# Optimization experiments

Hardware: AMD Instinct MI355X
Metric: run time of the kernel (lower is better)

## Reference

```python
import jax, jax.numpy as jnp
import numpy as np
import math

D_MODEL = 768
N_HEAD = 12
HEAD_DIM = D_MODEL // N_HEAD
B = 4
W = 32
HW = W * W


def setup_inputs() -> dict:
    key = jax.random.key(0)
    k1, k2, k3 = jax.random.split(key, 3)
    x = jax.random.normal(k1, (B, HW, D_MODEL), dtype=jnp.float32)
    w_qkv = jax.random.normal(k2, (3 * D_MODEL, D_MODEL), dtype=jnp.float32) * (D_MODEL ** -0.5)
    w_out = jax.random.normal(k3, (D_MODEL, D_MODEL), dtype=jnp.float32) * (D_MODEL ** -0.5)
    gamma = jnp.ones((D_MODEL,), dtype=jnp.float32)
    return {"x": x, "w_qkv": w_qkv, "w_out": w_out, "gamma": gamma}


def _axial_sincos(w, head_dim, dtype):
    # Axial RoPE: first half of head_dim encodes row position, second half column.
    dim_half = head_dim // 2
    inv_freq = 1.0 / (10000.0 ** (jnp.arange(0, dim_half, 2, dtype=dtype) / dim_half))  # (dim_half//2,)
    pos = jnp.arange(w, dtype=dtype)
    ang = pos[:, None] * inv_freq[None, :]                 # (w, f)
    row = jnp.repeat(ang[:, None, :], w, axis=1)           # (w, w, f)
    col = jnp.repeat(ang[None, :, :], w, axis=0)           # (w, w, f)
    theta = jnp.concatenate([row, col], axis=-1).reshape(w * w, dim_half)  # (hw, head_dim//2)
    theta = jnp.concatenate([theta, theta], axis=-1)       # rotate-half layout -> (hw, head_dim)
    return jnp.sin(theta), jnp.cos(theta)


def _rotate_half(t):
    t1, t2 = jnp.split(t, 2, axis=-1)
    return jnp.concatenate([-t2, t1], axis=-1)


def _apply_rotary(t, sin, cos):
    return t * cos + _rotate_half(t) * sin


def _rms_norm(x, gamma, eps=1e-6):
    return x * jax.lax.rsqrt(jnp.mean(x * x, axis=-1, keepdims=True) + eps) * gamma


def _attn_mask(w):
    # Faithful to the torch source: mask[center, neighbor] = False, else True.
    # torch SDPA bool semantics: True = attend. So 3x3 neighbors are EXCLUDED.
    idx = jnp.arange(w * w)
    r, c = idx // w, idx % w
    neighbor = (jnp.abs(r[:, None] - r[None, :]) <= 1) & (jnp.abs(c[:, None] - c[None, :]) <= 1)
    return ~neighbor  # (hw, hw) bool, True = allowed


def reference(x, w_qkv, w_out, gamma):
    Bx, hw, d = x.shape
    w = int(math.isqrt(hw))
    h, hd = N_HEAD, HEAD_DIM
    sin, cos = _axial_sincos(w, hd, x.dtype)               # (hw, hd) each
    xn = _rms_norm(x, gamma)
    qkv = xn @ w_qkv.T                                     # (B, hw, 3d)
    qkv = qkv.reshape(Bx, hw, 3, h, hd)
    q = jnp.transpose(qkv[:, :, 0], (0, 2, 1, 3))          # (B, h, hw, hd)
    k = jnp.transpose(qkv[:, :, 1], (0, 2, 1, 3))
    v = jnp.transpose(qkv[:, :, 2], (0, 2, 1, 3))
    q = _apply_rotary(q, sin, cos)
    k = _apply_rotary(k, sin, cos)
    allow = _attn_mask(w)
    scale = 1.0 / jnp.sqrt(jnp.asarray(hd, x.dtype))
    scores = jnp.einsum('bhid,bhjd->bhij', q, k) * scale   # (B, h, hw, hw)
    scores = jnp.where(allow[None, None], scores, jnp.asarray(-jnp.inf, x.dtype))
    probs = jax.nn.softmax(scores, axis=-1)
    out = jnp.einsum('bhij,bhjd->bhid', probs, v)          # (B, h, hw, hd)
    out = jnp.transpose(out, (0, 2, 1, 3)).reshape(Bx, hw, d)
    return out @ w_out.T
```

## Files before the change

kernel.cpp:

```cpp
#include <hip/hip_runtime.h>

typedef __attribute__((ext_vector_type(8))) short short8;
typedef __attribute__((ext_vector_type(4))) float f32x4;
typedef __attribute__((ext_vector_type(4))) unsigned short ushort4_t;
typedef unsigned short ushort_t;
typedef unsigned long long u64;

#define D_MODEL 768
#define NHEAD 12
#define HD 64
#define BATCH 4
#define HWIDTH 32
#define HW 1024
#define TOK (BATCH*HW)
#define QKV_N (3*D_MODEL)
#define BH (BATCH*NHEAD)
#define QSCALE 0.18033688f

__device__ __forceinline__ ushort_t f2bf(float f) {
    union { float f; unsigned u; } v; v.f = f;
    unsigned u = v.u;
    unsigned r = u + 0x7FFFu + ((u >> 16) & 1u);
    return (ushort_t)(r >> 16);
}
__device__ __forceinline__ float bf2f(ushort_t h) {
    union { unsigned u; float f; } v; v.u = ((unsigned)h) << 16;
    return v.f;
}
__device__ __forceinline__ float ex2(float x) {
    float r; asm("v_exp_f32 %0, %1" : "=v"(r) : "v"(x)); return r;
}
__device__ __forceinline__ unsigned cvtpk(float lo, float hi) {
    unsigned r; asm("v_cvt_pk_bf16_f32 %0, %1, %2" : "=v"(r) : "v"(lo), "v"(hi)); return r;
}

__global__ void rmsnorm_kernel(const float* __restrict__ x, const float* __restrict__ gamma,
                               ushort_t* __restrict__ xn) {
    int wave = threadIdx.x >> 6, lane = threadIdx.x & 63;
    int t = blockIdx.x * 4 + wave;
    const float* xr = x + (size_t)t * D_MODEL;
    float v[12]; float ss = 0.f;
    #pragma unroll
    for (int j = 0; j < 12; ++j) { v[j] = xr[lane + j*64]; ss += v[j]*v[j]; }
    #pragma unroll
    for (int m = 1; m < 64; m <<= 1) ss += __shfl_xor(ss, m, 64);
    float r = rsqrtf(ss * (1.f/768.f) + 1e-6f);
    ushort_t* o = xn + (size_t)t * D_MODEL;
    #pragma unroll
    for (int j = 0; j < 12; ++j) o[lane + j*64] = f2bf(v[j] * r * gamma[lane + j*64]);
}

__global__ void cvt_kernel(const float* __restrict__ in, ushort_t* __restrict__ out, int n) {
    int i = blockIdx.x * blockDim.x + threadIdx.x;
    if (i < n) out[i] = f2bf(in[i]);
}

__global__ void sincos_kernel(float* __restrict__ sint, float* __restrict__ cost) {
    int i = blockIdx.x * blockDim.x + threadIdx.x;
    int p = i >> 5, j = i & 31;
    int r = p >> 5, c = p & 31;
    int jj = j & 15;
    float freq = powf(10000.f, -(float)(2*jj) / 32.f);
    float pos = (j < 16) ? (float)r : (float)c;
    float th = pos * freq;
    sint[i] = sinf(th);
    cost[i] = cosf(th);
}

template<int NTILES, int EPI>
__global__ __launch_bounds__(256, 2) void gemm128(const ushort_t* __restrict__ A,
                                                  const ushort_t* __restrict__ B,
                                                  const float* __restrict__ sint,
                                                  const float* __restrict__ cost,
                                                  ushort_t* __restrict__ Qr,
                                                  ushort_t* __restrict__ Kr,
                                                  ushort_t* __restrict__ VTt,
                                                  float* __restrict__ C) {
    __shared__ ushort_t As[2][128*64];
    __shared__ ushort_t Bs[2][128*64];
    const int K = 768;
    constexpr int NR = NTILES / 2;
    int c = blockIdx.x & 7;
    int l = blockIdx.x >> 3;
    int mtile = (c >> 1)*8 + l / NR;
    int ntile = (c & 1)*NR + l % NR;
    int tm = mtile * 128, tn = ntile * 128;
    int w = threadIdx.x >> 6, lane = threadIdx.x & 63;
    int wr = w >> 1, wc = w & 1;
    int l15 = lane & 15, l4 = lane >> 4;

    const ushort_t* mat = (w < 2) ? A : B;
    int mbase = (w < 2) ? tm : tn;
    ushort_t* lds_half = (w < 2) ? &As[0][0] : &Bs[0][0];
    int r0w = (w & 1) * 64;
    int srow = r0w + (lane >> 3);
    int sslot = (lane & 7) ^ (srow & 7);
    const ushort_t* gsrc0 = mat + (size_t)(mbase + srow)*K + sslot*8;

    auto stage = [&](int buf, int kstep) {
        int k0 = kstep * 64;
        #pragma unroll
        for (int j = 0; j < 8; ++j) {
            const ushort_t* g = gsrc0 + (size_t)(j*8)*K + k0;
            __builtin_amdgcn_global_load_lds((const __attribute__((address_space(1))) void*)g,
                (__attribute__((address_space(3))) void*)(lds_half + (size_t)buf*8192 + (r0w + j*8)*64),
                16, 0, 0);
        }
    };

    f32x4 acc[4][4] = {};
    auto compute = [&](int bi) {
        short8 af[4][2], bfx[4][2];
        #pragma unroll
        for (int mi = 0; mi < 4; ++mi) {
            int row = wr*64 + mi*16 + l15;
            #pragma unroll
            for (int kk = 0; kk < 2; ++kk)
                af[mi][kk] = *(const short8*)&As[bi][row*64 + ((kk*4 + l4) ^ (row & 7))*8];
        }
        #pragma unroll
        for (int ni = 0; ni < 4; ++ni) {
            int row = wc*64 + ni*16 + l15;
            #pragma unroll
            for (int kk = 0; kk < 2; ++kk)
                bfx[ni][kk] = *(const short8*)&Bs[bi][row*64 + ((kk*4 + l4) ^ (row & 7))*8];
        }
        #pragma unroll
        for (int kk = 0; kk < 2; ++kk)
            #pragma unroll
            for (int mi = 0; mi < 4; ++mi)
                #pragma unroll
                for (int ni = 0; ni < 4; ++ni)
                    acc[mi][ni] = __builtin_amdgcn_mfma_f32_16x16x32_bf16(af[mi][kk], bfx[ni][kk], acc[mi][ni], 0, 0, 0);
    };

    stage(0, 0); stage(1, 1);
    for (int t = 0; t < 12; ++t) {
        if (t < 11) { asm volatile("s_waitcnt vmcnt(8)" ::: "memory"); }
        else        { asm volatile("s_waitcnt vmcnt(0)" ::: "memory"); }
        __builtin_amdgcn_s_barrier();
        compute(t & 1);
        __builtin_amdgcn_s_barrier();
        if (t < 10) stage(t & 1, t + 2);
    }

    if constexpr (EPI == 0) {
        int col_base = tn + wc*64;
        int region = col_base / 768;
        int h = (col_base % 768) >> 6;
        if (region < 2) {
            ushort_t* dst = (region == 0) ? Qr : Kr;
            float scale = (region == 0) ? QSCALE : 1.f;
            #pragma unroll
            for (int mi = 0; mi < 4; ++mi) {
                #pragma unroll
                for (int ni = 0; ni < 2; ++ni) {
                    int d = ni*16 + l15;
                    #pragma unroll
                    for (int r = 0; r < 4; ++r) {
                        int pt = tm + wr*64 + mi*16 + l4*4 + r;
                        int b = pt >> 10, p = pt & 1023;
                        float s = sint[p*32 + d], cc = cost[p*32 + d];
                        float t0 = acc[mi][ni][r], t1 = acc[mi][ni+2][r];
                        size_t o = (size_t)(b*NHEAD + h)*HW*HD + (size_t)p*HD + d;
                        dst[o]      = f2bf((t0*cc - t1*s) * scale);
                        dst[o + 32] = f2bf((t1*cc + t0*s) * scale);
                    }
                }
            }
        } else {
            #pragma unroll
            for (int mi = 0; mi < 4; ++mi) {
                int pt = tm + wr*64 + mi*16 + l4*4;
                int b = pt >> 10, p = pt & 1023;
                size_t hb = (size_t)(b*NHEAD + h)*HD*HW;
                #pragma unroll
                for (int ni = 0; ni < 4; ++ni) {
                    int d = ni*16 + l15;
                    ushort4_t pk;
                    pk.x = f2bf(acc[mi][ni][0]);
                    pk.y = f2bf(acc[mi][ni][1]);
                    pk.z = f2bf(acc[mi][ni][2]);
                    pk.w = f2bf(acc[mi][ni][3]);
                    *(ushort4_t*)&VTt[hb + (size_t)d*HW + p] = pk;
                }
            }
        }
    } else {
        #pragma unroll
        for (int mi = 0; mi < 4; ++mi)
            #pragma unroll
            for (int ni = 0; ni < 4; ++ni)
                #pragma unroll
                for (int r = 0; r < 4; ++r) {
                    int row = tm + wr*64 + mi*16 + l4*4 + r;
                    int col = tn + wc*64 + ni*16 + l15;
                    C[(size_t)row*(128*NTILES) + col] = acc[mi][ni][r];
                }
    }
}

__global__ __launch_bounds__(256) void attn_kernel(const ushort_t* __restrict__ Q,
                                                   const ushort_t* __restrict__ Kt,
                                                   const ushort_t* __restrict__ VT,
                                                   ushort_t* __restrict__ Ao) {
    __shared__ ushort_t Kb[2][64*64];
    __shared__ ushort_t Vb[2][64*64];
    __shared__ ushort_t P[4][16][72];
    int flat = blockIdx.x;
    int swz = (flat & 7) * 96 + (flat >> 3);
    int bh = swz >> 4;
    int qtile = swz & 15;
    int w = threadIdx.x >> 6, lane = threadIdx.x & 63;
    int l15 = lane & 15, l4 = lane >> 4;
    int qbase = qtile * 64 + w * 16;
    int q = qbase + l15;
    int qr = q >> 5, qc = q & 31;
    const ushort_t* Qh = Q + (size_t)bh * HW * HD;
    const ushort_t* Kh = Kt + (size_t)bh * HW * HD;
    const ushort_t* Vh = VT + (size_t)bh * HD * HW;
    short8 aq0 = *(const short8*)&Qh[(size_t)q*64 + l4*8];
    short8 aq1 = *(const short8*)&Qh[(size_t)q*64 + 32 + l4*8];
    unsigned pat = (qc == 0) ? 3u : (7u << (qc - 1));
    float m = -1e30f, lsum = 0.f;
    f32x4 oacc[4] = {};

    auto stage = [&](int bufi, int kv) {
        #pragma unroll
        for (int is = 0; is < 2; ++is) {
            int c = is*256 + w*64 + lane;
            int row = c >> 3;
            int col16 = (c & 7) ^ (row & 7);
            const ushort_t* ga = Kh + (size_t)(kv + row)*64 + col16*8;
            __builtin_amdgcn_global_load_lds((const __attribute__((address_space(1))) void*)ga,
                (__attribute__((address_space(3))) void*)(&Kb[bufi][(size_t)(is*256 + w*64)*8]), 16, 0, 0);
            const ushort_t* gv = Vh + (size_t)row*HW + kv + col16*8;
            __builtin_amdgcn_global_load_lds((const __attribute__((address_space(1))) void*)gv,
                (__attribute__((address_space(3))) void*)(&Vb[bufi][(size_t)(is*256 + w*64)*8]), 16, 0, 0);
        }
    };

    stage(0, 0); stage(1, 64);

    for (int t = 0; t < 16; ++t) {
        if (t < 15) { asm volatile("s_waitcnt vmcnt(4)" ::: "memory"); }
        else        { asm volatile("s_waitcnt vmcnt(0)" ::: "memory"); }
        __builtin_amdgcn_s_barrier();
        int cur = t & 1;
        int kv = t * 64;
        int sw = l15 & 7;
        f32x4 s[4];
        #pragma unroll
        for (int st = 0; st < 4; ++st) {
            int krow = st*16 + l15;
            short8 bk0 = *(const short8*)&Kb[cur][(size_t)krow*64 + (size_t)((l4 ^ sw))*8];
            short8 bk1 = *(const short8*)&Kb[cur][(size_t)krow*64 + (size_t)(((4+l4) ^ sw))*8];
            f32x4 z = {};
            z = __builtin_amdgcn_mfma_f32_16x16x32_bf16(bk0, aq0, z, 0, 0, 0);
            z = __builtin_amdgcn_mfma_f32_16x16x32_bf16(bk1, aq1, z, 0, 0, 0);
            s[st] = z;
        }
        short8 va0[4], va1[4];
        #pragma unroll
        for (int dt = 0; dt < 4; ++dt) {
            int vrow = dt*16 + l15;
            va0[dt] = *(const short8*)&Vb[cur][(size_t)vrow*64 + (size_t)((l4 ^ sw))*8];
            va1[dt] = *(const short8*)&Vb[cur][(size_t)vrow*64 + (size_t)(((4+l4) ^ sw))*8];
        }
        int dr = qr - (kv >> 5);
        if (dr >= -1 && dr <= 2) {
            u64 tm = 0;
            if (dr <= 1) tm |= (u64)pat;
            if (dr >= 0) tm |= ((u64)pat) << 32;
            u64 sub = tm >> (l4*4);
            #pragma unroll
            for (int st = 0; st < 4; ++st)
                #pragma unroll
                for (int i = 0; i < 4; ++i)
                    if ((sub >> (st*16 + i)) & 1) s[st][i] = -1e30f;
        }
        float vmax = fmaxf(
            fmaxf(fmaxf(fmaxf(s[0][0], s[0][1]), fmaxf(s[0][2], s[0][3])),
                  fmaxf(fmaxf(s[1][0], s[1][1]), fmaxf(s[1][2], s[1][3]))),
            fmaxf(fmaxf(fmaxf(s[2][0], s[2][1]), fmaxf(s[2][2], s[2][3])),
                  fmaxf(fmaxf(s[3][0], s[3][1]), fmaxf(s[3][2], s[3][3]))));
        vmax = fmaxf(vmax, __shfl_xor(vmax, 16, 64));
        vmax = fmaxf(vmax, __shfl_xor(vmax, 32, 64));
        if (__any(vmax - m > 8.f)) {
            float mn = fmaxf(m, vmax);
            float sf = ex2(m - mn);
            lsum *= sf;
            #pragma unroll
            for (int dt = 0; dt < 4; ++dt)
                #pragma unroll
                for (int i = 0; i < 4; ++i) oacc[dt][i] *= sf;
            m = mn;
        }
        float ls = 0.f;
        #pragma unroll
        for (int st = 0; st < 4; ++st) {
            float p0 = ex2(s[st][0] - m), p1 = ex2(s[st][1] - m);
            float p2 = ex2(s[st][2] - m), p3 = ex2(s[st][3] - m);
            ls += (p0 + p1) + (p2 + p3);
            uint2 pk;
            pk.x = cvtpk(p0, p1);
            pk.y = cvtpk(p2, p3);
            *(uint2*)&P[w][l15][st*16 + l4*4] = pk;
        }
        ls += __shfl_xor(ls, 16, 64);
        ls += __shfl_xor(ls, 32, 64);
        lsum += ls;
        short8 pf0 = *(const short8*)&P[w][l15][l4*8];
        short8 pf1 = *(const short8*)&P[w][l15][32 + l4*8];
        #pragma unroll
        for (int dt = 0; dt < 4; ++dt) {
            oacc[dt] = __builtin_amdgcn_mfma_f32_16x16x32_bf16(va0[dt], pf0, oacc[dt], 0, 0, 0);
            oacc[dt] = __builtin_amdgcn_mfma_f32_16x16x32_bf16(va1[dt], pf1, oacc[dt], 0, 0, 0);
        }
        __builtin_amdgcn_s_barrier();
        if (t < 14) stage(cur, (t + 2) * 64);
    }
    int b = bh / NHEAD, h = bh % NHEAD;
    float rl = 1.f / lsum;
    size_t obase = ((size_t)b*HW + q)*D_MODEL + h*64;
    #pragma unroll
    for (int dt = 0; dt < 4; ++dt) {
        uint2 pk;
        pk.x = cvtpk(oacc[dt][0]*rl, oacc[dt][1]*rl);
        pk.y = cvtpk(oacc[dt][2]*rl, oacc[dt][3]*rl);
        *(uint2*)&Ao[obase + dt*16 + l4*4] = pk;
    }
}

extern "C" void kernel_launch(void* const* d_in, const int* in_sizes, int n_in,
                              void* d_out, int out_size, void* d_ws, size_t ws_size,
                              hipStream_t stream) {
    const float* x      = (const float*)d_in[0];
    const float* w_qkv  = (const float*)d_in[1];
    const float* w_out  = (const float*)d_in[2];
    const float* gamma  = (const float*)d_in[3];
    float* out = (float*)d_out;

    char* ws = (char*)d_ws;
    size_t off = 0;
    auto alloc = [&](size_t bytes) { char* p = ws + off; off += (bytes + 255) & ~255ull; return p; };
    ushort_t* xn   = (ushort_t*)alloc((size_t)TOK*D_MODEL*2);
    ushort_t* wq   = (ushort_t*)alloc((size_t)QKV_N*D_MODEL*2);
    ushort_t* wo   = (ushort_t*)alloc((size_t)D_MODEL*D_MODEL*2);
    float* sint    = (float*)alloc((size_t)HW*32*4);
    float* cost    = (float*)alloc((size_t)HW*32*4);
    ushort_t* Qr   = (ushort_t*)alloc((size_t)BH*HW*HD*2);
    ushort_t* Kr   = (ushort_t*)alloc((size_t)BH*HW*HD*2);
    ushort_t* VTt  = (ushort_t*)alloc((size_t)BH*HD*HW*2);
    ushort_t* Ao   = (ushort_t*)alloc((size_t)TOK*D_MODEL*2);

    rmsnorm_kernel<<<TOK/4, 256, 0, stream>>>(x, gamma, xn);
    cvt_kernel<<<(QKV_N*D_MODEL + 255)/256, 256, 0, stream>>>(w_qkv, wq, QKV_N*D_MODEL);
    cvt_kernel<<<(D_MODEL*D_MODEL + 255)/256, 256, 0, stream>>>(w_out, wo, D_MODEL*D_MODEL);
    sincos_kernel<<<HW*32/256, 256, 0, stream>>>(sint, cost);
    gemm128<18,0><<<576, 256, 0, stream>>>(xn, wq, sint, cost, Qr, Kr, VTt, nullptr);
    attn_kernel<<<768, 256, 0, stream>>>(Qr, Kr, VTt, Ao);
    gemm128<6,1><<<192, 256, 0, stream>>>(Ao, wo, nullptr, nullptr, nullptr, nullptr, nullptr, out);
}
```

Measured before the change: 80.10 us.

## Split attention KV into two halves with combine pass, fuse prep kernels, reorder GEMM pipeline

Merges the rmsnorm, weight-conversion and sincos kernels into one prep launch, with float4-vectorised weight conversion. Attention is now split over two halves of the key range, each using 32-key tiles, and a new combine kernel merges the partial outputs and (max, sum) pairs. This doubles the block count and raises occupancy through smaller LDS tiles and launch_bounds(256,6), and adds setprio around the MFMAs. The GEMM and attention loops now read their LDS fragments first, then issue the next prefetch before the MFMAs to overlap loads with compute. The cost is extra fp32 partial traffic and one more kernel launch.

After: 82.22 us. 2.6% more time.

```diff
diff --git a/kernel.cpp b/kernel.cpp
--- a/kernel.cpp
+++ b/kernel.cpp
@@ -4,7 +4,6 @@
 typedef __attribute__((ext_vector_type(4))) float f32x4;
 typedef __attribute__((ext_vector_type(4))) unsigned short ushort4_t;
 typedef unsigned short ushort_t;
-typedef unsigned long long u64;
 
 #define D_MODEL 768
 #define NHEAD 12
@@ -23,10 +22,6 @@
     unsigned r = u + 0x7FFFu + ((u >> 16) & 1u);
     return (ushort_t)(r >> 16);
 }
-__device__ __forceinline__ float bf2f(ushort_t h) {
-    union { unsigned u; float f; } v; v.u = ((unsigned)h) << 16;
-    return v.f;
-}
 __device__ __forceinline__ float ex2(float x) {
     float r; asm("v_exp_f32 %0, %1" : "=v"(r) : "v"(x)); return r;
 }
@@ -34,37 +29,50 @@
     unsigned r; asm("v_cvt_pk_bf16_f32 %0, %1, %2" : "=v"(r) : "v"(lo), "v"(hi)); return r;
 }
 
-__global__ void rmsnorm_kernel(const float* __restrict__ x, const float* __restrict__ gamma,
-                               ushort_t* __restrict__ xn) {
-    int wave = threadIdx.x >> 6, lane = threadIdx.x & 63;
-    int t = blockIdx.x * 4 + wave;
-    const float* xr = x + (size_t)t * D_MODEL;
-    float v[12]; float ss = 0.f;
-    #pragma unroll
-    for (int j = 0; j < 12; ++j) { v[j] = xr[lane + j*64]; ss += v[j]*v[j]; }
-    #pragma unroll
-    for (int m = 1; m < 64; m <<= 1) ss += __shfl_xor(ss, m, 64);
-    float r = rsqrtf(ss * (1.f/768.f) + 1e-6f);
-    ushort_t* o = xn + (size_t)t * D_MODEL;
-    #pragma unroll
-    for (int j = 0; j < 12; ++j) o[lane + j*64] = f2bf(v[j] * r * gamma[lane + j*64]);
-}
-
-__global__ void cvt_kernel(const float* __restrict__ in, ushort_t* __restrict__ out, int n) {
-    int i = blockIdx.x * blockDim.x + threadIdx.x;
-    if (i < n) out[i] = f2bf(in[i]);
-}
-
-__global__ void sincos_kernel(float* __restrict__ sint, float* __restrict__ cost) {
-    int i = blockIdx.x * blockDim.x + threadIdx.x;
-    int p = i >> 5, j = i & 31;
-    int r = p >> 5, c = p & 31;
-    int jj = j & 15;
-    float freq = powf(10000.f, -(float)(2*jj) / 32.f);
-    float pos = (j < 16) ? (float)r : (float)c;
-    float th = pos * freq;
-    sint[i] = sinf(th);
-    cost[i] = cosf(th);
+__global__ __launch_bounds__(256) void prep_kernel(const float* __restrict__ x,
+                                                   const float* __restrict__ gamma,
+                                                   ushort_t* __restrict__ xn,
+                                                   const float* __restrict__ w_qkv,
+                                                   ushort_t* __restrict__ wq,
+                                                   const float* __restrict__ w_out,
+                                                   ushort_t* __restrict__ wo,
+                                                   float* __restrict__ sint,
+                                                   float* __restrict__ cost) {
+    int blk = blockIdx.x;
+    if (blk < 1024) {
+        int wave = threadIdx.x >> 6, lane = threadIdx.x & 63;
+        int t = blk * 4 + wave;
+        const float* xr = x + (size_t)t * D_MODEL;
+        float v[12]; float ss = 0.f;
+        #pragma unroll
+        for (int j = 0; j < 12; ++j) { v[j] = xr[lane + j*64]; ss += v[j]*v[j]; }
+        #pragma unroll
+        for (int m = 1; m < 64; m <<= 1) ss += __shfl_xor(ss, m, 64);
+        float r = rsqrtf(ss * (1.f/768.f) + 1e-6f);
+        ushort_t* o = xn + (size_t)t * D_MODEL;
+        #pragma unroll
+        for (int j = 0; j < 12; ++j) o[lane + j*64] = f2bf(v[j] * r * gamma[lane + j*64]);
+    } else if (blk < 2752) {
+        int i = (blk - 1024) * 1024 + threadIdx.x * 4;
+        float4 v = *(const float4*)&w_qkv[i];
+        uint2 pk; pk.x = cvtpk(v.x, v.y); pk.y = cvtpk(v.z, v.w);
+        *(uint2*)&wq[i] = pk;
+    } else if (blk < 3328) {
+        int i = (blk - 2752) * 1024 + threadIdx.x * 4;
+        float4 v = *(const float4*)&w_out[i];
+        uint2 pk; pk.x = cvtpk(v.x, v.y); pk.y = cvtpk(v.z, v.w);
+        *(uint2*)&wo[i] = pk;
+    } else {
+        int i = (blk - 3328) * 256 + threadIdx.x;
+        int p = i >> 5, j = i & 31;
+        int r = p >> 5, c = p & 31;
+        int jj = j & 15;
+        float freq = powf(10000.f, -(float)(2*jj) / 32.f);
+        float pos = (j < 16) ? (float)r : (float)c;
+        float th = pos * freq;
+        sint[i] = sinf(th);
+        cost[i] = cosf(th);
+    }
 }
 
 template<int NTILES, int EPI>
@@ -109,39 +117,37 @@
     };
 
     f32x4 acc[4][4] = {};
-    auto compute = [&](int bi) {
-        short8 af[4][2], bfx[4][2];
-        #pragma unroll
-        for (int mi = 0; mi < 4; ++mi) {
-            int row = wr*64 + mi*16 + l15;
-            #pragma unroll
-            for (int kk = 0; kk < 2; ++kk)
-                af[mi][kk] = *(const short8*)&As[bi][row*64 + ((kk*4 + l4) ^ (row & 7))*8];
-        }
-        #pragma unroll
-        for (int ni = 0; ni < 4; ++ni) {
-            int row = wc*64 + ni*16 + l15;
-            #pragma unroll
-            for (int kk = 0; kk < 2; ++kk)
-                bfx[ni][kk] = *(const short8*)&Bs[bi][row*64 + ((kk*4 + l4) ^ (row & 7))*8];
-        }
-        #pragma unroll
-        for (int kk = 0; kk < 2; ++kk)
-            #pragma unroll
-            for (int mi = 0; mi < 4; ++mi)
-                #pragma unroll
-                for (int ni = 0; ni < 4; ++ni)
-                    acc[mi][ni] = __builtin_amdgcn_mfma_f32_16x16x32_bf16(af[mi][kk], bfx[ni][kk], acc[mi][ni], 0, 0, 0);
-    };
-
     stage(0, 0); stage(1, 1);
     for (int t = 0; t < 12; ++t) {
         if (t < 11) { asm volatile("s_waitcnt vmcnt(8)" ::: "memory"); }
         else        { asm volatile("s_waitcnt vmcnt(0)" ::: "memory"); }
         __builtin_amdgcn_s_barrier();
-        compute(t & 1);
+        int bi = t & 1;
+        short8 af[4][2], bfx[4][2];
+        #pragma unroll
+        for (int mi = 0; mi < 4; ++mi) {
+            int row = wr*64 + mi*16 + l15;
+            #pragma unroll
+            for (int kk = 0; kk < 2; ++kk)
+                af[mi][kk] = *(const short8*)&As[bi][row*64 + ((kk*4 + l4) ^ (row & 7))*8];
+        }
+        #pragma unroll
+        for (int ni = 0; ni < 4; ++ni) {
+            int row = wc*64 + ni*16 + l15;
+            #pragma unroll
+            for (int kk = 0; kk < 2; ++kk)
+                bfx[ni][kk] = *(const short8*)&Bs[bi][row*64 + ((kk*4 + l4) ^ (row & 7))*8];
+        }
+        asm volatile("s_waitcnt lgkmcnt(0)" ::: "memory");
         __builtin_amdgcn_s_barrier();
-        if (t < 10) stage(t & 1, t + 2);
+        if (t < 10) stage(bi, t + 2);
+        #pragma unroll
+        for (int kk = 0; kk < 2; ++kk)
+            #pragma unroll
+            for (int mi = 0; mi < 4; ++mi)
+                #pragma unroll
+                for (int ni = 0; ni < 4; ++ni)
+                    acc[mi][ni] = __builtin_amdgcn_mfma_f32_16x16x32_bf16(af[mi][kk], bfx[ni][kk], acc[mi][ni], 0, 0, 0);
     }
 
     if constexpr (EPI == 0) {
@@ -200,22 +206,21 @@
     }
 }
 
-__global__ __launch_bounds__(256) void attn_kernel(const ushort_t* __restrict__ Q,
-                                                   const ushort_t* __restrict__ Kt,
-                                                   const ushort_t* __restrict__ VT,
-                                                   ushort_t* __restrict__ Ao) {
-    __shared__ ushort_t Kb[2][64*64];
-    __shared__ ushort_t Vb[2][64*64];
-    __shared__ ushort_t P[4][16][72];
-    int flat = blockIdx.x;
-    int swz = (flat & 7) * 96 + (flat >> 3);
-    int bh = swz >> 4;
-    int qtile = swz & 15;
+__global__ __launch_bounds__(256, 6) void attn_kernel(const ushort_t* __restrict__ Q,
+                                                      const ushort_t* __restrict__ Kt,
+                                                      const ushort_t* __restrict__ VT,
+                                                      float* __restrict__ Opart,
+                                                      float2* __restrict__ Ml) {
+    __shared__ ushort_t Kb[2][32*64];
+    __shared__ ushort_t Vb[2][64*32];
+    __shared__ ushort_t P[4][16][40];
+    int qtile = blockIdx.x, bh = blockIdx.y, split = blockIdx.z;
     int w = threadIdx.x >> 6, lane = threadIdx.x & 63;
     int l15 = lane & 15, l4 = lane >> 4;
     int qbase = qtile * 64 + w * 16;
     int q = qbase + l15;
-    int qr = q >> 5, qc = q & 31;
+    int qr = qbase >> 5;
+    int qc = q & 31;
     const ushort_t* Qh = Q + (size_t)bh * HW * HD;
     const ushort_t* Kh = Kt + (size_t)bh * HW * HD;
     const ushort_t* Vh = VT + (size_t)bh * HD * HW;
@@ -224,66 +229,67 @@
     unsigned pat = (qc == 0) ? 3u : (7u << (qc - 1));
     float m = -1e30f, lsum = 0.f;
     f32x4 oacc[4] = {};
-
+    int kv0 = split * 512;
+
+    int krow_s = w*8 + (lane >> 3);
+    int kslot_s = (lane & 7) ^ (lane >> 3);
+    int vrow_s = w*16 + (lane >> 2);
+    int vslot_s = (lane & 3) ^ (vrow_s & 3) ^ ((vrow_s >> 2) & 3);
     auto stage = [&](int bufi, int kv) {
-        #pragma unroll
-        for (int is = 0; is < 2; ++is) {
-            int c = is*256 + w*64 + lane;
-            int row = c >> 3;
-            int col16 = (c & 7) ^ (row & 7);
-            const ushort_t* ga = Kh + (size_t)(kv + row)*64 + col16*8;
-            __builtin_amdgcn_global_load_lds((const __attribute__((address_space(1))) void*)ga,
-                (__attribute__((address_space(3))) void*)(&Kb[bufi][(size_t)(is*256 + w*64)*8]), 16, 0, 0);
-            const ushort_t* gv = Vh + (size_t)row*HW + kv + col16*8;
-            __builtin_amdgcn_global_load_lds((const __attribute__((address_space(1))) void*)gv,
-                (__attribute__((address_space(3))) void*)(&Vb[bufi][(size_t)(is*256 + w*64)*8]), 16, 0, 0);
-        }
+        const ushort_t* ga = Kh + (size_t)(kv + krow_s)*64 + kslot_s*8;
+        __builtin_amdgcn_global_load_lds((const __attribute__((address_space(1))) void*)ga,
+            (__attribute__((address_space(3))) void*)(&Kb[bufi][w*512]), 16, 0, 0);
+        const ushort_t* gv = Vh + (size_t)vrow_s*HW + kv + vslot_s*8;
+        __builtin_amdgcn_global_load_lds((const __attribute__((address_space(1))) void*)gv,
+            (__attribute__((address_space(3))) void*)(&Vb[bufi][w*512]), 16, 0, 0);
     };
 
-    stage(0, 0); stage(1, 64);
+    stage(0, kv0); stage(1, kv0 + 32);
 
     for (int t = 0; t < 16; ++t) {
-        if (t < 15) { asm volatile("s_waitcnt vmcnt(4)" ::: "memory"); }
+        if (t < 15) { asm volatile("s_waitcnt vmcnt(2)" ::: "memory"); }
         else        { asm volatile("s_waitcnt vmcnt(0)" ::: "memory"); }
         __builtin_amdgcn_s_barrier();
         int cur = t & 1;
-        int kv = t * 64;
-        int sw = l15 & 7;
-        f32x4 s[4];
-        #pragma unroll
-        for (int st = 0; st < 4; ++st) {
+        int kv = kv0 + t * 32;
+        short8 bk[2][2];
+        #pragma unroll
+        for (int st = 0; st < 2; ++st) {
             int krow = st*16 + l15;
-            short8 bk0 = *(const short8*)&Kb[cur][(size_t)krow*64 + (size_t)((l4 ^ sw))*8];
-            short8 bk1 = *(const short8*)&Kb[cur][(size_t)krow*64 + (size_t)(((4+l4) ^ sw))*8];
-            f32x4 z = {};
-            z = __builtin_amdgcn_mfma_f32_16x16x32_bf16(bk0, aq0, z, 0, 0, 0);
-            z = __builtin_amdgcn_mfma_f32_16x16x32_bf16(bk1, aq1, z, 0, 0, 0);
-            s[st] = z;
-        }
-        short8 va0[4], va1[4];
+            bk[st][0] = *(const short8*)&Kb[cur][krow*64 + ((l4 ^ (krow & 7)))*8];
+            bk[st][1] = *(const short8*)&Kb[cur][krow*64 + (((4 + l4) ^ (krow & 7)))*8];
+        }
+        short8 va[4];
         #pragma unroll
         for (int dt = 0; dt < 4; ++dt) {
             int vrow = dt*16 + l15;
-            va0[dt] = *(const short8*)&Vb[cur][(size_t)vrow*64 + (size_t)((l4 ^ sw))*8];
-            va1[dt] = *(const short8*)&Vb[cur][(size_t)vrow*64 + (size_t)(((4+l4) ^ sw))*8];
-        }
+            va[dt] = *(const short8*)&Vb[cur][vrow*32 + ((l4 ^ (vrow & 3) ^ ((vrow >> 2) & 3)))*8];
+        }
+        asm volatile("s_waitcnt lgkmcnt(0)" ::: "memory");
+        __builtin_amdgcn_s_barrier();
+        if (t < 14) stage(cur, kv0 + (t + 2) * 32);
+        f32x4 s[2];
+        __builtin_amdgcn_s_setprio(1);
+        #pragma unroll
+        for (int st = 0; st < 2; ++st) {
+            f32x4 z = {};
+            z = __builtin_amdgcn_mfma_f32_16x16x32_bf16(bk[st][0], aq0, z, 0, 0, 0);
+            z = __builtin_amdgcn_mfma_f32_16x16x32_bf16(bk[st][1], aq1, z, 0, 0, 0);
+            s[st] = z;
+        }
+        __builtin_amdgcn_s_setprio(0);
         int dr = qr - (kv >> 5);
-        if (dr >= -1 && dr <= 2) {
-            u64 tm = 0;
-            if (dr <= 1) tm |= (u64)pat;
-            if (dr >= 0) tm |= ((u64)pat) << 32;
-            u64 sub = tm >> (l4*4);
-            #pragma unroll
-            for (int st = 0; st < 4; ++st)
+        if (dr >= -1 && dr <= 1) {
+            unsigned sub = pat >> (l4*4);
+            #pragma unroll
+            for (int st = 0; st < 2; ++st)
                 #pragma unroll
                 for (int i = 0; i < 4; ++i)
                     if ((sub >> (st*16 + i)) & 1) s[st][i] = -1e30f;
         }
         float vmax = fmaxf(
-            fmaxf(fmaxf(fmaxf(s[0][0], s[0][1]), fmaxf(s[0][2], s[0][3])),
-                  fmaxf(fmaxf(s[1][0], s[1][1]), fmaxf(s[1][2], s[1][3]))),
-            fmaxf(fmaxf(fmaxf(s[2][0], s[2][1]), fmaxf(s[2][2], s[2][3])),
-                  fmaxf(fmaxf(s[3][0], s[3][1]), fmaxf(s[3][2], s[3][3]))));
+            fmaxf(fmaxf(s[0][0], s[0][1]), fmaxf(s[0][2], s[0][3])),
+            fmaxf(fmaxf(s[1][0], s[1][1]), fmaxf(s[1][2], s[1][3])));
         vmax = fmaxf(vmax, __shfl_xor(vmax, 16, 64));
         vmax = fmaxf(vmax, __shfl_xor(vmax, 32, 64));
         if (__any(vmax - m > 8.f)) {
@@ -298,38 +304,45 @@
         }
         float ls = 0.f;
         #pragma unroll
-        for (int st = 0; st < 4; ++st) {
+        for (int st = 0; st < 2; ++st) {
             float p0 = ex2(s[st][0] - m), p1 = ex2(s[st][1] - m);
             float p2 = ex2(s[st][2] - m), p3 = ex2(s[st][3] - m);
             ls += (p0 + p1) + (p2 + p3);
-            uint2 pk;
-            pk.x = cvtpk(p0, p1);
-            pk.y = cvtpk(p2, p3);
+            uint2 pk; pk.x = cvtpk(p0, p1); pk.y = cvtpk(p2, p3);
             *(uint2*)&P[w][l15][st*16 + l4*4] = pk;
         }
         ls += __shfl_xor(ls, 16, 64);
         ls += __shfl_xor(ls, 32, 64);
         lsum += ls;
-        short8 pf0 = *(const short8*)&P[w][l15][l4*8];
-        short8 pf1 = *(const short8*)&P[w][l15][32 + l4*8];
-        #pragma unroll
-        for (int dt = 0; dt < 4; ++dt) {
-            oacc[dt] = __builtin_amdgcn_mfma_f32_16x16x32_bf16(va0[dt], pf0, oacc[dt], 0, 0, 0);
-            oacc[dt] = __builtin_amdgcn_mfma_f32_16x16x32_bf16(va1[dt], pf1, oacc[dt], 0, 0, 0);
-        }
-        __builtin_amdgcn_s_barrier();
-        if (t < 14) stage(cur, (t + 2) * 64);
+        short8 pf = *(const short8*)&P[w][l15][l4*8];
+        __builtin_amdgcn_s_setprio(1);
+        #pragma unroll
+        for (int dt = 0; dt < 4; ++dt)
+            oacc[dt] = __builtin_amdgcn_mfma_f32_16x16x32_bf16(va[dt], pf, oacc[dt], 0, 0, 0);
+        __builtin_amdgcn_s_setprio(0);
     }
+    size_t rowid = (size_t)(split*BH + bh) * HW + q;
+    #pragma unroll
+    for (int dt = 0; dt < 4; ++dt)
+        *(f32x4*)&Opart[rowid*64 + dt*16 + l4*4] = oacc[dt];
+    if (l4 == 0) Ml[rowid] = make_float2(m, lsum);
+}
+
+__global__ void combine_kernel(const float* __restrict__ Opart, const float2* __restrict__ Ml,
+                               ushort_t* __restrict__ Ao) {
+    int w = threadIdx.x >> 6, lane = threadIdx.x & 63;
+    int row = blockIdx.x * 4 + w;
+    int bh = row >> 10, q = row & 1023;
     int b = bh / NHEAD, h = bh % NHEAD;
-    float rl = 1.f / lsum;
-    size_t obase = ((size_t)b*HW + q)*D_MODEL + h*64;
-    #pragma unroll
-    for (int dt = 0; dt < 4; ++dt) {
-        uint2 pk;
-        pk.x = cvtpk(oacc[dt][0]*rl, oacc[dt][1]*rl);
-        pk.y = cvtpk(oacc[dt][2]*rl, oacc[dt][3]*rl);
-        *(uint2*)&Ao[obase + dt*16 + l4*4] = pk;
-    }
+    float2 ml1 = Ml[row];
+    float2 ml2 = Ml[(size_t)BH*HW + row];
+    float mm = fmaxf(ml1.x, ml2.x);
+    float e1 = ex2(ml1.x - mm), e2 = ex2(ml2.x - mm);
+    float denom = e1*ml1.y + e2*ml2.y;
+    float o1 = Opart[(size_t)row*64 + lane];
+    float o2 = Opart[((size_t)BH*HW + row)*64 + lane];
+    float o = (e1*o1 + e2*o2) / denom;
+    Ao[((size_t)b*HW + q)*D_MODEL + h*64 + lane] = f2bf(o);
 }
 
 extern "C" void kernel_launch(void* const* d_in, const int* in_sizes, int n_in,
@@ -353,12 +366,12 @@
     ushort_t* Kr   = (ushort_t*)alloc((size_t)BH*HW*HD*2);
     ushort_t* VTt  = (ushort_t*)alloc((size_t)BH*HD*HW*2);
     ushort_t* Ao   = (ushort_t*)alloc((size_t)TOK*D_MODEL*2);
-
-    rmsnorm_kernel<<<TOK/4, 256, 0, stream>>>(x, gamma, xn);
-    cvt_kernel<<<(QKV_N*D_MODEL + 255)/256, 256, 0, stream>>>(w_qkv, wq, QKV_N*D_MODEL);
-    cvt_kernel<<<(D_MODEL*D_MODEL + 255)/256, 256, 0, stream>>>(w_out, wo, D_MODEL*D_MODEL);
-    sincos_kernel<<<HW*32/256, 256, 0, stream>>>(sint, cost);
+    float* Opart   = (float*)alloc((size_t)2*BH*HW*64*4);
+    float2* Ml     = (float2*)alloc((size_t)2*BH*HW*8);
+
+    prep_kernel<<<3456, 256, 0, stream>>>(x, gamma, xn, w_qkv, wq, w_out, wo, sint, cost);
     gemm128<18,0><<<576, 256, 0, stream>>>(xn, wq, sint, cost, Qr, Kr, VTt, nullptr);
-    attn_kernel<<<768, 256, 0, stream>>>(Qr, Kr, VTt, Ao);
+    attn_kernel<<<dim3(16, 48, 2), 256, 0, stream>>>(Qr, Kr, VTt, Opart, Ml);
+    combine_kernel<<<BH*HW/4, 256, 0, stream>>>(Opart, Ml, Ao);
     gemm128<6,1><<<192, 256, 0, stream>>>(Ao, wo, nullptr, nullptr, nullptr, nullptr, nullptr, out);
 }
```

## Merge prep kernels into one launch and load attention K/V directly to registers

Applied to the files above, without the earlier changes.

Four preprocessing launches (rmsnorm, two weight conversions, sincos) become one prep kernel dispatched by block index, and the weight conversion is vectorised to float4. The attention kernel drops its LDS double-buffered K/V staging and barriers and instead loads K fragments (prefetched one tile ahead) and V fragments straight from global memory into registers. It also raises scheduling priority around the MFMA blocks and asks for 3 blocks per CU. This removes launch overhead and barrier syncs, at the cost of uncoalesced, unshared global loads that every wave repeats and that may not hide latency.

Result: slower. 130.0 us (+62.3%).

```diff
diff --git a/kernel.cpp b/kernel.cpp
--- a/kernel.cpp
+++ b/kernel.cpp
@@ -23,10 +23,6 @@
     unsigned r = u + 0x7FFFu + ((u >> 16) & 1u);
     return (ushort_t)(r >> 16);
 }
-__device__ __forceinline__ float bf2f(ushort_t h) {
-    union { unsigned u; float f; } v; v.u = ((unsigned)h) << 16;
-    return v.f;
-}
 __device__ __forceinline__ float ex2(float x) {
     float r; asm("v_exp_f32 %0, %1" : "=v"(r) : "v"(x)); return r;
 }
@@ -34,37 +30,50 @@
     unsigned r; asm("v_cvt_pk_bf16_f32 %0, %1, %2" : "=v"(r) : "v"(lo), "v"(hi)); return r;
 }
 
-__global__ void rmsnorm_kernel(const float* __restrict__ x, const float* __restrict__ gamma,
-                               ushort_t* __restrict__ xn) {
-    int wave = threadIdx.x >> 6, lane = threadIdx.x & 63;
-    int t = blockIdx.x * 4 + wave;
-    const float* xr = x + (size_t)t * D_MODEL;
-    float v[12]; float ss = 0.f;
-    #pragma unroll
-    for (int j = 0; j < 12; ++j) { v[j] = xr[lane + j*64]; ss += v[j]*v[j]; }
-    #pragma unroll
-    for (int m = 1; m < 64; m <<= 1) ss += __shfl_xor(ss, m, 64);
-    float r = rsqrtf(ss * (1.f/768.f) + 1e-6f);
-    ushort_t* o = xn + (size_t)t * D_MODEL;
-    #pragma unroll
-    for (int j = 0; j < 12; ++j) o[lane + j*64] = f2bf(v[j] * r * gamma[lane + j*64]);
-}
-
-__global__ void cvt_kernel(const float* __restrict__ in, ushort_t* __restrict__ out, int n) {
-    int i = blockIdx.x * blockDim.x + threadIdx.x;
-    if (i < n) out[i] = f2bf(in[i]);
-}
-
-__global__ void sincos_kernel(float* __restrict__ sint, float* __restrict__ cost) {
-    int i = blockIdx.x * blockDim.x + threadIdx.x;
-    int p = i >> 5, j = i & 31;
-    int r = p >> 5, c = p & 31;
-    int jj = j & 15;
-    float freq = powf(10000.f, -(float)(2*jj) / 32.f);
-    float pos = (j < 16) ? (float)r : (float)c;
-    float th = pos * freq;
-    sint[i] = sinf(th);
-    cost[i] = cosf(th);
+__global__ __launch_bounds__(256) void prep_kernel(const float* __restrict__ x,
+                                                   const float* __restrict__ gamma,
+                                                   ushort_t* __restrict__ xn,
+                                                   const float* __restrict__ w_qkv,
+                                                   ushort_t* __restrict__ wq,
+                                                   const float* __restrict__ w_out,
+                                                   ushort_t* __restrict__ wo,
+                                                   float* __restrict__ sint,
+                                                   float* __restrict__ cost) {
+    int blk = blockIdx.x;
+    if (blk < 1024) {
+        int wave = threadIdx.x >> 6, lane = threadIdx.x & 63;
+        int t = blk * 4 + wave;
+        const float* xr = x + (size_t)t * D_MODEL;
+        float v[12]; float ss = 0.f;
+        #pragma unroll
+        for (int j = 0; j < 12; ++j) { v[j] = xr[lane + j*64]; ss += v[j]*v[j]; }
+        #pragma unroll
+        for (int m = 1; m < 64; m <<= 1) ss += __shfl_xor(ss, m, 64);
+        float r = rsqrtf(ss * (1.f/768.f) + 1e-6f);
+        ushort_t* o = xn + (size_t)t * D_MODEL;
+        #pragma unroll
+        for (int j = 0; j < 12; ++j) o[lane + j*64] = f2bf(v[j] * r * gamma[lane + j*64]);
+    } else if (blk < 2752) {
+        int i = (blk - 1024) * 1024 + threadIdx.x * 4;
+        float4 v = *(const float4*)&w_qkv[i];
+        uint2 pk; pk.x = cvtpk(v.x, v.y); pk.y = cvtpk(v.z, v.w);
+        *(uint2*)&wq[i] = pk;
+    } else if (blk < 3328) {
+        int i = (blk - 2752) * 1024 + threadIdx.x * 4;
+        float4 v = *(const float4*)&w_out[i];
+        uint2 pk; pk.x = cvtpk(v.x, v.y); pk.y = cvtpk(v.z, v.w);
+        *(uint2*)&wo[i] = pk;
+    } else {
+        int i = (blk - 3328) * 256 + threadIdx.x;
+        int p = i >> 5, j = i & 31;
+        int r = p >> 5, c = p & 31;
+        int jj = j & 15;
+        float freq = powf(10000.f, -(float)(2*jj) / 32.f);
+        float pos = (j < 16) ? (float)r : (float)c;
+        float th = pos * freq;
+        sint[i] = sinf(th);
+        cost[i] = cosf(th);
+    }
 }
 
 template<int NTILES, int EPI>
@@ -200,12 +209,10 @@
     }
 }
 
-__global__ __launch_bounds__(256) void attn_kernel(const ushort_t* __restrict__ Q,
-                                                   const ushort_t* __restrict__ Kt,
-                                                   const ushort_t* __restrict__ VT,
-                                                   ushort_t* __restrict__ Ao) {
-    __shared__ ushort_t Kb[2][64*64];
-    __shared__ ushort_t Vb[2][64*64];
+__global__ __launch_bounds__(256, 3) void attn_kernel(const ushort_t* __restrict__ Q,
+                                                      const ushort_t* __restrict__ Kt,
+                                                      const ushort_t* __restrict__ VT,
+                                                      ushort_t* __restrict__ Ao) {
     __shared__ ushort_t P[4][16][72];
     int flat = blockIdx.x;
     int swz = (flat & 7) * 96 + (flat >> 3);
@@ -225,47 +232,37 @@
     float m = -1e30f, lsum = 0.f;
     f32x4 oacc[4] = {};
 
-    auto stage = [&](int bufi, int kv) {
-        #pragma unroll
-        for (int is = 0; is < 2; ++is) {
-            int c = is*256 + w*64 + lane;
-            int row = c >> 3;
-            int col16 = (c & 7) ^ (row & 7);
-            const ushort_t* ga = Kh + (size_t)(kv + row)*64 + col16*8;
-            __builtin_amdgcn_global_load_lds((const __attribute__((address_space(1))) void*)ga,
-                (__attribute__((address_space(3))) void*)(&Kb[bufi][(size_t)(is*256 + w*64)*8]), 16, 0, 0);
-            const ushort_t* gv = Vh + (size_t)row*HW + kv + col16*8;
-            __builtin_amdgcn_global_load_lds((const __attribute__((address_space(1))) void*)gv,
-                (__attribute__((address_space(3))) void*)(&Vb[bufi][(size_t)(is*256 + w*64)*8]), 16, 0, 0);
-        }
-    };
-
-    stage(0, 0); stage(1, 64);
+    short8 kf[4][2];
+    #pragma unroll
+    for (int st = 0; st < 4; ++st) {
+        kf[st][0] = *(const short8*)&Kh[(size_t)(st*16 + l15)*64 + l4*8];
+        kf[st][1] = *(const short8*)&Kh[(size_t)(st*16 + l15)*64 + 32 + l4*8];
+    }
 
     for (int t = 0; t < 16; ++t) {
-        if (t < 15) { asm volatile("s_waitcnt vmcnt(4)" ::: "memory"); }
-        else        { asm volatile("s_waitcnt vmcnt(0)" ::: "memory"); }
-        __builtin_amdgcn_s_barrier();
-        int cur = t & 1;
         int kv = t * 64;
-        int sw = l15 & 7;
+        short8 va[4][2];
+        #pragma unroll
+        for (int dt = 0; dt < 4; ++dt) {
+            va[dt][0] = *(const short8*)&Vh[(size_t)(dt*16 + l15)*HW + kv + l4*8];
+            va[dt][1] = *(const short8*)&Vh[(size_t)(dt*16 + l15)*HW + kv + 32 + l4*8];
+        }
         f32x4 s[4];
+        __builtin_amdgcn_s_setprio(1);
         #pragma unroll
         for (int st = 0; st < 4; ++st) {
-            int krow = st*16 + l15;
-            short8 bk0 = *(const short8*)&Kb[cur][(size_t)krow*64 + (size_t)((l4 ^ sw))*8];
-            short8 bk1 = *(const short8*)&Kb[cur][(size_t)krow*64 + (size_t)(((4+l4) ^ sw))*8];
             f32x4 z = {};
-            z = __builtin_amdgcn_mfma_f32_16x16x32_bf16(bk0, aq0, z, 0, 0, 0);
-            z = __builtin_amdgcn_mfma_f32_16x16x32_bf16(bk1, aq1, z, 0, 0, 0);
+            z = __builtin_amdgcn_mfma_f32_16x16x32_bf16(kf[st][0], aq0, z, 0, 0, 0);
+            z = __builtin_amdgcn_mfma_f32_16x16x32_bf16(kf[st][1], aq1, z, 0, 0, 0);
             s[st] = z;
         }
-        short8 va0[4], va1[4];
-        #pragma unroll
-        for (int dt = 0; dt < 4; ++dt) {
-            int vrow = dt*16 + l15;
-            va0[dt] = *(const short8*)&Vb[cur][(size_t)vrow*64 + (size_t)((l4 ^ sw))*8];
-            va1[dt] = *(const short8*)&Vb[cur][(size_t)vrow*64 + (size_t)(((4+l4) ^ sw))*8];
+        __builtin_amdgcn_s_setprio(0);
+        if (t < 15) {
+            #pragma unroll
+            for (int st = 0; st < 4; ++st) {
+                kf[st][0] = *(const short8*)&Kh[(size_t)(kv + 64 + st*16 + l15)*64 + l4*8];
+                kf[st][1] = *(const short8*)&Kh[(size_t)(kv + 64 + st*16 + l15)*64 + 32 + l4*8];
+            }
         }
         int dr = qr - (kv >> 5);
         if (dr >= -1 && dr <= 2) {
@@ -312,13 +309,13 @@
         lsum += ls;
         short8 pf0 = *(const short8*)&P[w][l15][l4*8];
         short8 pf1 = *(const short8*)&P[w][l15][32 + l4*8];
+        __builtin_amdgcn_s_setprio(1);
         #pragma unroll
         for (int dt = 0; dt < 4; ++dt) {
-            oacc[dt] = __builtin_amdgcn_mfma_f32_16x16x32_bf16(va0[dt], pf0, oacc[dt], 0, 0, 0);
-            oacc[dt] = __builtin_amdgcn_mfma_f32_16x16x32_bf16(va1[dt], pf1, oacc[dt], 0, 0, 0);
-        }
-        __builtin_amdgcn_s_barrier();
-        if (t < 14) stage(cur, (t + 2) * 64);
+            oacc[dt] = __builtin_amdgcn_mfma_f32_16x16x32_bf16(va[dt][0], pf0, oacc[dt], 0, 0, 0);
+            oacc[dt] = __builtin_amdgcn_mfma_f32_16x16x32_bf16(va[dt][1], pf1, oacc[dt], 0, 0, 0);
+        }
+        __builtin_amdgcn_s_setprio(0);
     }
     int b = bh / NHEAD, h = bh % NHEAD;
     float rl = 1.f / lsum;
@@ -354,10 +351,7 @@
     ushort_t* VTt  = (ushort_t*)alloc((size_t)BH*HD*HW*2);
     ushort_t* Ao   = (ushort_t*)alloc((size_t)TOK*D_MODEL*2);
 
-    rmsnorm_kernel<<<TOK/4, 256, 0, stream>>>(x, gamma, xn);
-    cvt_kernel<<<(QKV_N*D_MODEL + 255)/256, 256, 0, stream>>>(w_qkv, wq, QKV_N*D_MODEL);
-    cvt_kernel<<<(D_MODEL*D_MODEL + 255)/256, 256, 0, stream>>>(w_out, wo, D_MODEL*D_MODEL);
-    sincos_kernel<<<HW*32/256, 256, 0, stream>>>(sint, cost);
+    prep_kernel<<<3456, 256, 0, stream>>>(x, gamma, xn, w_qkv, wq, w_out, wo, sint, cost);
     gemm128<18,0><<<576, 256, 0, stream>>>(xn, wq, sint, cost, Qr, Kr, VTt, nullptr);
     attn_kernel<<<768, 256, 0, stream>>>(Qr, Kr, VTt, Ao);
     gemm128<6,1><<<192, 256, 0, stream>>>(Ao, wo, nullptr, nullptr, nullptr, nullptr, nullptr, out);
```
